# Kernel tuning notes

Measured on AMD Instinct MI355X. Metric: run time of the kernel, lower is better.

The kernel has to match this reference:

```python
import jax, jax.numpy as jnp
import numpy as np

B, T, H, C = 16, 6000, 256, 105
NOTE_BD_TEMP = 1.0
THRESH = 0.5
MIN_GAP = 19      # round(100 * 24000 / 1000 / 128)
REF_GAP = 9       # round(50 * 24000 / 1000 / 128)


def setup_inputs() -> dict:
    key = jax.random.key(0)
    kf, kw = jax.random.split(key)
    feat = jax.random.normal(kf, (B, T, H), dtype=jnp.float32)
    # kaiming normal fan_in: std = sqrt(2/fan_in)
    W = jax.random.normal(kw, (C, H), dtype=jnp.float32) * np.float32(np.sqrt(2.0 / H))
    b = jnp.zeros((C,), dtype=jnp.float32)
    rng = np.random.default_rng(0)
    word_bd = np.zeros((B, T), dtype=np.int32)
    for i in range(B):
        pos = np.cumsum(rng.integers(25, 61, size=T // 25)) + 10
        pos = pos[pos < T - 2]
        word_bd[i, pos] = 1
    lengths = rng.integers(T // 2, T + 1, size=B)
    non_padding = (np.arange(T)[None, :] < lengths[:, None]).astype(np.float32)
    return {"feat": feat, "word_bd": jnp.asarray(word_bd),
            "non_padding": jnp.asarray(non_padding), "W": W, "b": b}


def _phase1(probs, bd):
    # Peak-picking + min-gap merging scan over one sequence.
    # probs, bd: [T]. Returns res: [T+1] int32 (slot T is a dummy write sink).
    def step(carry, inp):
        res, last, start, rmv, rmi = carry
        j, bj, pj = inp
        in_run = start >= 0
        upd = (~in_run) | (pj > rmv)          # running first-argmax of current run
        fin = (~bj) & in_run                  # run just ended at j
        bd_idx = rmi                          # argmax index of the run (== start if len 1)
        merge = fin & (bd_idx - last < MIN_GAP) & (last > 0)
        mid = jnp.round((bd_idx + last).astype(jnp.float32) / 2.0).astype(jnp.int32)
        bd_idx = jnp.where(merge, mid, bd_idx)
        res = res.at[jnp.where(merge, last, T)].set(0)
        res = res.at[jnp.where(fin, bd_idx, T)].set(1)
        last = jnp.where(fin, bd_idx, last)
        start = jnp.where(bj, jnp.where(in_run, start, j), jnp.where(fin, -1, start))
        rmv = jnp.where(bj & upd, pj, rmv)
        rmi = jnp.where(bj & upd, j, rmi)
        return (res, last, start, rmv, rmi), None

    init = (jnp.zeros((T + 1,), jnp.int32), jnp.int32(-1), jnp.int32(-1),
            jnp.float32(-1e30), jnp.int32(0))
    xs = (jnp.arange(T, dtype=jnp.int32), bd, probs)
    (res, _, _, _, _), _ = jax.lax.scan(step, init, xs)
    return res


def _phase2(res, ref):
    # Reconcile predicted boundaries with reference word boundaries.
    ds = jnp.arange(-REF_GAP, REF_GAP)        # window [j-g, j+g-1] == torch slice [j-g : j+g]
    ks = jnp.arange(1, REF_GAP + 1)

    def step(res, j):
        active = ref[j] == 1
        widx = j + ds
        valid = (widx >= 0) & (widx < T)
        cwidx = jnp.clip(widx, 0, T - 1)
        seg = jnp.sum(jnp.where(valid, res[cwidx], 0))
        b0 = seg == 0
        b1 = (seg == 1) & (res[j] != 1)
        b2 = seg > 1
        # branch seg>1: first (in l1,r1,l2,r2,... order) offending boundary to suppress
        lidx = jnp.maximum(0, j - ks)
        ridx = jnp.minimum(T - 1, j + ks)
        cl = (res[lidx] == 1) & (ref[lidx] != 1)
        cr = (res[ridx] == 1) & (ref[ridx] != 1)
        conds = jnp.stack([cl, cr], axis=1).reshape(-1)
        cands = jnp.stack([lidx, ridx], axis=1).reshape(-1)
        zidx = jnp.where(jnp.any(conds), cands[jnp.argmax(conds)], T)
        # apply branch effects (inactive writes go to dummy slot T)
        res = res.at[jnp.where(active & b1 & valid, widx, T)].set(ref[cwidx])
        res = res.at[jnp.where(active & b2, zidx, T)].set(0)
        res = res.at[jnp.where(active & (b0 | b2), j, T)].set(1)
        return res, None

    res, _ = jax.lax.scan(step, res, jnp.arange(T, dtype=jnp.int32))
    return res


def regulate_boundary(bd_logits, word_bd, non_padding):
    probs = jax.nn.sigmoid(bd_logits)
    bd = probs > THRESH
    res = jax.vmap(_phase1)(probs, bd)
    res = jax.vmap(_phase2)(res, word_bd)
    res = res[:, :T]                      # drop dummy slot
    res = res.at[:, 0].set(0)
    L = jnp.sum(non_padding, axis=1).astype(jnp.int32)   # [B]
    keep = jnp.arange(T)[None, :] < (L[:, None] - 1)     # zero out res[i, L-1:]
    return jnp.where(keep, res, 0)


def reference(feat, word_bd, non_padding, W, b):
    # note_head: Linear(H -> C); eval mode so dropout is identity
    logits = jnp.einsum('bth,ch->btc', feat, W) + b           # [B,T,C]
    note_bd_logits = jnp.clip(logits[:, :, 0] / NOTE_BD_TEMP, -16.0, 16.0)
    note_frame_logits = logits[:, :, 1:] / NOTE_BD_TEMP
    note_bd_pred = regulate_boundary(note_bd_logits, word_bd, non_padding)
    return note_bd_logits, note_frame_logits, note_bd_pred
```

## Files before the change

kernel.cpp:

```cpp
#include <hip/hip_runtime.h>

#define NB 16
#define TT 6000
#define HH 256
#define CC 105
#define MIN_GAP_ 19
#define REF_GAP_ 9

using short8  = __attribute__((ext_vector_type(8))) short;
using short4v = __attribute__((ext_vector_type(4))) short;
using f32x4   = __attribute__((ext_vector_type(4))) float;

static __device__ __forceinline__ short f2bf(float x) {
  unsigned u = __builtin_bit_cast(unsigned, x);
  unsigned r = (u + 0x7FFFu + ((u >> 16) & 1u)) >> 16;
  return (short)r;
}

__global__ __launch_bounds__(256) void wconv_kernel(
    const float* __restrict__ W, unsigned short* __restrict__ Wb) {
  const int idx = blockIdx.x * 256 + threadIdx.x;
  const int c = idx >> 8, k = idx & 255;
  const float v = (c < CC - 1) ? W[(size_t)(c + 1) * HH + k] : 0.f;
  Wb[idx] = (unsigned short)f2bf(v);
}

__global__ __launch_bounds__(512, 4) void gemm_mfma(
    const float* __restrict__ feat, const float* __restrict__ W,
    const float* __restrict__ bias, const unsigned short* __restrict__ Wb,
    float* __restrict__ out0, float* __restrict__ out1) {
  __shared__ __align__(16) unsigned short bS[112 * 256];
  const int tid  = threadIdx.x;
  const int wv   = tid >> 6;
  const int lane = tid & 63;
  const int rl   = lane & 15;
  const int kg   = lane >> 4;
  const int row  = blockIdx.x * 128 + wv * 16 + rl;
  const float* frow = feat + (size_t)row * HH;

  short8 breg[7];
#pragma unroll
  for (int i = 0; i < 7; i++)
    breg[i] = *reinterpret_cast<const short8*>(Wb + (((size_t)(i * 512 + tid)) << 3));

  float4 areg[16];
#pragma unroll
  for (int ks = 0; ks < 8; ks++) {
    const int kk = ks * 32 + kg * 8;
    areg[2 * ks]     = *reinterpret_cast<const float4*>(frow + kk);
    areg[2 * ks + 1] = *reinterpret_cast<const float4*>(frow + kk + 4);
  }

#pragma unroll
  for (int i = 0; i < 7; i++) {
    const int byte = (i * 512 + tid) << 4;
    const int brow = byte >> 9;
    const int boff = byte & 511;
    *reinterpret_cast<short8*>(
        (char*)bS + (brow << 9) + (boff ^ ((brow & 7) << 4))) = breg[i];
  }
  __syncthreads();

  const int xr = (rl & 7) << 4;
  f32x4 acc[7];
#pragma unroll
  for (int n = 0; n < 7; n++) acc[n] = (f32x4){0.f, 0.f, 0.f, 0.f};
  float c0 = 0.f;

#pragma unroll
  for (int ks = 0; ks < 8; ks++) {
    const int kk = ks * 32 + kg * 8;
    const float4 a0 = areg[2 * ks];
    const float4 a1 = areg[2 * ks + 1];
    const float4 w0a = *reinterpret_cast<const float4*>(W + kk);
    const float4 w0b = *reinterpret_cast<const float4*>(W + kk + 4);
    c0 = fmaf(a0.x, w0a.x, c0); c0 = fmaf(a0.y, w0a.y, c0);
    c0 = fmaf(a0.z, w0a.z, c0); c0 = fmaf(a0.w, w0a.w, c0);
    c0 = fmaf(a1.x, w0b.x, c0); c0 = fmaf(a1.y, w0b.y, c0);
    c0 = fmaf(a1.z, w0b.z, c0); c0 = fmaf(a1.w, w0b.w, c0);

    short8 av;
    av[0] = f2bf(a0.x); av[1] = f2bf(a0.y); av[2] = f2bf(a0.z); av[3] = f2bf(a0.w);
    av[4] = f2bf(a1.x); av[5] = f2bf(a1.y); av[6] = f2bf(a1.z); av[7] = f2bf(a1.w);

    const int boff = (ks * 64 + kg * 16) ^ xr;
    const char* bbase = (const char*)bS + boff;
    short8 bv[7];
#pragma unroll
    for (int n = 0; n < 7; n++)
      bv[n] = *reinterpret_cast<const short8*>(bbase + ((n * 16 + rl) << 9));
#pragma unroll
    for (int n = 0; n < 7; n++)
      acc[n] = __builtin_amdgcn_mfma_f32_16x16x32_bf16(av, bv[n], acc[n], 0, 0, 0);
  }

  c0 += __shfl_xor(c0, 16);
  c0 += __shfl_xor(c0, 32);
  if (kg == 0) out0[row] = fminf(fmaxf(c0 + bias[0], -16.f), 16.f);

  const int rbase = blockIdx.x * 128 + wv * 16 + kg * 4;
#pragma unroll
  for (int n = 0; n < 7; n++) {
    const int c = n * 16 + rl;
    if (c < CC - 1) {
      const float bb = bias[c + 1];
#pragma unroll
      for (int r = 0; r < 4; r++)
        out1[(size_t)(rbase + r) * (CC - 1) + c] = acc[n][r] + bb;
    }
  }
}

#define NW 192
#define NW_LAST 187
#define CHUNK 32
#define NCLS 19
#define MAXRUNS 3072
#define MAXCH 96

__global__ __launch_bounds__(512) void phase_kernel(
    const float* __restrict__ bd_logits,
    const int* __restrict__ word_bd,
    const float* __restrict__ non_padding,
    float* __restrict__ out2) {
  __shared__ __align__(16) float lbuf[TT];
  __shared__ unsigned char wbuf[TT];
  __shared__ int res[TT];
  __shared__ unsigned bdbits[NW];
  __shared__ int runIdx[MAXRUNS];
  __shared__ int outLast[MAXCH][NCLS + 1];
  __shared__ int chP0[MAXCH];
  __shared__ int inL[MAXCH + 1];
  __shared__ int wsum[8];
  __shared__ int wbase[8];
  __shared__ int L_sh, nruns_sh;

  const int b = blockIdx.x;
  const int tid = threadIdx.x;
  const int lane = tid & 63;
  const int wid = tid >> 6;
  if (tid == 0) L_sh = 0;
  __syncthreads();

  int cnt_np = 0;
#pragma unroll
  for (int k = 0; k < 12; k++) {
    const int j = k * 512 + tid;
    bool pred = false;
    if (j < TT) {
      const float l = bd_logits[(size_t)b * TT + j];
      lbuf[j] = l;
      pred = l > 0.f;
      wbuf[j] = (unsigned char)word_bd[(size_t)b * TT + j];
      res[j] = 0;
      cnt_np += (non_padding[(size_t)b * TT + j] != 0.f) ? 1 : 0;
    }
    const unsigned long long m = __ballot(pred);
    if (lane == 0) {
      const int w0 = (k * 512 + (tid & ~63)) >> 5;
      bdbits[w0]     = (unsigned)m;
      bdbits[w0 + 1] = (unsigned)(m >> 32);
    }
  }
#pragma unroll
  for (int off = 32; off; off >>= 1) cnt_np += __shfl_xor(cnt_np, off);
  if (lane == 0) atomicAdd(&L_sh, cnt_np);
  __syncthreads();

  int cnt = 0;
  unsigned ends = 0;
  if (tid < NW) {
    const unsigned cur = bdbits[tid];
    const unsigned pb = tid ? (bdbits[tid - 1] >> 31) : 0u;
    ends = ((cur << 1) | pb) & ~cur;
    if (tid == NW_LAST) ends &= 0xFFFFu;
    cnt = __popc(ends);
  }
  int v = cnt;
#pragma unroll
  for (int off = 1; off < 64; off <<= 1) {
    const int t = __shfl_up(v, off);
    if (lane >= off) v += t;
  }
  if (lane == 63) wsum[wid] = v;
  __syncthreads();
  if (tid == 0) {
    int s = 0;
#pragma unroll
    for (int w = 0; w < 8; w++) { wbase[w] = s; s += wsum[w]; }
    nruns_sh = s;
  }
  __syncthreads();
  int slot = wbase[wid] + v - cnt;

  if (ends) {
    unsigned m = ends;
    while (m) {
      const int bit = __builtin_ctz(m);
      m &= m - 1;
      const int e = tid * 32 + bit;
      const int eb = e - 1;
      int w = eb >> 5;
      const int bb = eb & 31;
      const unsigned z = bdbits[w] << (31 - bb);
      const unsigned nz = ~z;
      int run = nz ? __builtin_clz(nz) : 32;
      if (run == bb + 1) {
        while (w > 0) {
          w--;
          const unsigned nx = ~bdbits[w];
          const int t2 = nx ? __builtin_clz(nx) : 32;
          run += t2;
          if (t2 < 32) break;
        }
      }
      const int s = e - run;
      float mv = lbuf[s];
      int mi = s;
      for (int i = s + 1; i < e; i++) {
        const float val = lbuf[i];
        if (val > mv) { mv = val; mi = i; }
      }
      runIdx[slot++] = mi;
    }
  }
  __syncthreads();

  const int n = nruns_sh;
  const int nch = (n + CHUNK - 1) / CHUNK;
  for (int f = tid; f < nch * NCLS; f += 512) {
    const int ch = f / NCLS;
    const int cls = f - ch * NCLS;
    const int s = ch * CHUNK;
    const int e = (s + CHUNK < n) ? s + CHUNK : n;
    const int p0 = runIdx[s];
    if (cls == NCLS - 1) chP0[ch] = p0;
    int last = (cls < 18) ? (p0 - 18 + cls) : -1;
    for (int i = s; i < e; i++) {
      int bd = runIdx[i];
      if (last > 0 && bd - last < MIN_GAP_) {
        const int sum = bd + last;
        const int h = sum >> 1;
        bd = (sum & 1) ? (h + (h & 1)) : h;
      }
      last = bd;
    }
    outLast[ch][cls] = last;
  }
  __syncthreads();

  if (wid == 0) {
    int q = -1;
    int row = (lane < NCLS && nch > 0) ? outLast[0][lane] : -1;
    for (int ch = 0; ch < nch; ch++) {
      const int rown = (lane < NCLS && ch + 1 < nch) ? outLast[ch + 1][lane] : -1;
      const int p0 = chP0[ch];
      const int cls = (q > 0 && p0 - q < MIN_GAP_) ? (q - (p0 - 18)) : (NCLS - 1);
      if (lane == 0) inL[ch] = q;
      q = __shfl(row, cls);
      row = rown;
    }
    if (lane == 0) inL[nch] = q;
  }
  __syncthreads();

  for (int ch = tid; ch < nch; ch += 512) {
    const int s = ch * CHUNK;
    const int e = (s + CHUNK < n) ? s + CHUNK : n;
    const int qin = inL[ch];
    const int qout = inL[ch + 1];
    if (qin >= 0 && qin != qout) res[qin] = 1;
    int last = qin;
    for (int i = s; i < e; i++) {
      int bd = runIdx[i];
      if (last > 0 && bd - last < MIN_GAP_) {
        const int sum = bd + last;
        const int h = sum >> 1;
        bd = (sum & 1) ? (h + (h & 1)) : h;
        if (last != qout) res[last] = 0;
      }
      if (bd != qout) res[bd] = 1;
      last = bd;
    }
  }
  if (tid == 0 && n > 0) res[inL[nch]] = 1;
  __syncthreads();

  for (int j = tid; j < TT; j += 512) {
    if (wbuf[j] != 1) continue;
    const int lo = (j - REF_GAP_ < 0) ? 0 : j - REF_GAP_;
    const int hi = (j + REF_GAP_ - 1 > TT - 1) ? TT - 1 : j + REF_GAP_ - 1;
    int seg = 0;
    for (int w = lo; w <= hi; w++) seg += res[w];
    if (seg == 0) {
      res[j] = 1;
    } else if (seg == 1) {
      if (res[j] != 1) {
        for (int w = lo; w <= hi; w++) res[w] = (int)wbuf[w];
      }
    } else {
      int zidx = -1;
      for (int k = 1; k <= REF_GAP_; k++) {
        const int li = (j - k < 0) ? 0 : j - k;
        const int ri = (j + k > TT - 1) ? TT - 1 : j + k;
        if (res[li] == 1 && wbuf[li] != 1) { zidx = li; break; }
        if (res[ri] == 1 && wbuf[ri] != 1) { zidx = ri; break; }
      }
      if (zidx >= 0) res[zidx] = 0;
      res[j] = 1;
    }
  }
  __syncthreads();

  const int L = L_sh;
  for (int t = tid; t < TT; t += 512)
    out2[(size_t)b * TT + t] = (t >= 1 && t < L - 1) ? (float)res[t] : 0.f;
}

extern "C" void kernel_launch(void* const* d_in, const int* in_sizes, int n_in,
                              void* d_out, int out_size, void* d_ws, size_t ws_size,
                              hipStream_t stream) {
  const float* feat        = (const float*)d_in[0];
  const int*   word_bd     = (const int*)d_in[1];
  const float* non_padding = (const float*)d_in[2];
  const float* W           = (const float*)d_in[3];
  const float* bias        = (const float*)d_in[4];

  float* out  = (float*)d_out;
  float* out0 = out;
  float* out1 = out + (size_t)NB * TT;
  float* out2 = out + (size_t)NB * TT + (size_t)NB * TT * (CC - 1);

  unsigned short* Wb = (unsigned short*)d_ws;

  hipLaunchKernelGGL(wconv_kernel, dim3(112), dim3(256), 0, stream, W, Wb);
  hipLaunchKernelGGL(gemm_mfma, dim3((NB * TT) / 128), dim3(512), 0, stream,
                     feat, W, bias, Wb, out0, out1);
  hipLaunchKernelGGL(phase_kernel, dim3(NB), dim3(512), 0, stream,
                     out0, word_bd, non_padding, out2);
}
```

Measured before the change: 69.67 us.

## Widen phase kernel to 1024 threads and map merge chunks to wavefronts

The phase kernel now runs 1024 threads per block. The chunked merge scans assign one wavefront per chunk: the chunk's run indices are loaded into lanes once and broadcast with shuffles, instead of every thread rereading shared memory serially. The intent is to cut shared-memory latency in the serial chunk loops and spread the load/refine loops across more threads. The GEMM grid is written as a named constant equal to the old value, so that part is cosmetic. In exchange, each chunk's sequential loop now runs in lockstep across a full wavefront, and a 1024-thread block may be limited in register use.

After: 81.84 us. +17.5%, slower.

```diff
diff --git a/kernel.cpp b/kernel.cpp
--- a/kernel.cpp
+++ b/kernel.cpp
@@ -24,6 +24,8 @@
   const float v = (c < CC - 1) ? W[(size_t)(c + 1) * HH + k] : 0.f;
   Wb[idx] = (unsigned short)f2bf(v);
 }
+
+#define NGRID 750
 
 __global__ __launch_bounds__(512, 4) void gemm_mfma(
     const float* __restrict__ feat, const float* __restrict__ W,
@@ -118,7 +120,7 @@
 #define MAXRUNS 3072
 #define MAXCH 96
 
-__global__ __launch_bounds__(512) void phase_kernel(
+__global__ __launch_bounds__(1024) void phase_kernel(
     const float* __restrict__ bd_logits,
     const int* __restrict__ word_bd,
     const float* __restrict__ non_padding,
@@ -131,21 +133,21 @@
   __shared__ int outLast[MAXCH][NCLS + 1];
   __shared__ int chP0[MAXCH];
   __shared__ int inL[MAXCH + 1];
-  __shared__ int wsum[8];
-  __shared__ int wbase[8];
+  __shared__ int wsum[16];
+  __shared__ int wbase[16];
   __shared__ int L_sh, nruns_sh;
 
   const int b = blockIdx.x;
   const int tid = threadIdx.x;
   const int lane = tid & 63;
-  const int wid = tid >> 6;
+  const int wv = tid >> 6;
   if (tid == 0) L_sh = 0;
   __syncthreads();
 
   int cnt_np = 0;
 #pragma unroll
-  for (int k = 0; k < 12; k++) {
-    const int j = k * 512 + tid;
+  for (int k = 0; k < 6; k++) {
+    const int j = k * 1024 + tid;
     bool pred = false;
     if (j < TT) {
       const float l = bd_logits[(size_t)b * TT + j];
@@ -157,7 +159,7 @@
     }
     const unsigned long long m = __ballot(pred);
     if (lane == 0) {
-      const int w0 = (k * 512 + (tid & ~63)) >> 5;
+      const int w0 = (k * 1024 + (tid & ~63)) >> 5;
       bdbits[w0]     = (unsigned)m;
       bdbits[w0 + 1] = (unsigned)(m >> 32);
     }
@@ -182,16 +184,16 @@
     const int t = __shfl_up(v, off);
     if (lane >= off) v += t;
   }
-  if (lane == 63) wsum[wid] = v;
+  if (lane == 63) wsum[wv] = v;
   __syncthreads();
   if (tid == 0) {
     int s = 0;
 #pragma unroll
-    for (int w = 0; w < 8; w++) { wbase[w] = s; s += wsum[w]; }
+    for (int w = 0; w < 16; w++) { wbase[w] = s; s += wsum[w]; }
     nruns_sh = s;
   }
   __syncthreads();
-  int slot = wbase[wid] + v - cnt;
+  int slot = wbase[wv] + v - cnt;
 
   if (ends) {
     unsigned m = ends;
@@ -228,16 +230,16 @@
 
   const int n = nruns_sh;
   const int nch = (n + CHUNK - 1) / CHUNK;
-  for (int f = tid; f < nch * NCLS; f += 512) {
-    const int ch = f / NCLS;
-    const int cls = f - ch * NCLS;
+  for (int ch = wv; ch < nch; ch += 16) {
     const int s = ch * CHUNK;
     const int e = (s + CHUNK < n) ? s + CHUNK : n;
-    const int p0 = runIdx[s];
-    if (cls == NCLS - 1) chP0[ch] = p0;
-    int last = (cls < 18) ? (p0 - 18 + cls) : -1;
-    for (int i = s; i < e; i++) {
-      int bd = runIdx[i];
+    const int m = e - s;
+    const int myrun = (lane < m) ? runIdx[s + lane] : 0;
+    const int p0 = __shfl(myrun, 0);
+    if (lane == 0) chP0[ch] = p0;
+    int last = (lane < 18) ? (p0 - 18 + lane) : -1;
+    for (int i = 0; i < m; i++) {
+      int bd = __shfl(myrun, i);
       if (last > 0 && bd - last < MIN_GAP_) {
         const int sum = bd + last;
         const int h = sum >> 1;
@@ -245,11 +247,11 @@
       }
       last = bd;
     }
-    outLast[ch][cls] = last;
-  }
-  __syncthreads();
-
-  if (wid == 0) {
+    if (lane < NCLS) outLast[ch][lane] = last;
+  }
+  __syncthreads();
+
+  if (wv == 0) {
     int q = -1;
     int row = (lane < NCLS && nch > 0) ? outLast[0][lane] : -1;
     for (int ch = 0; ch < nch; ch++) {
@@ -264,29 +266,32 @@
   }
   __syncthreads();
 
-  for (int ch = tid; ch < nch; ch += 512) {
+  for (int ch = wv; ch < nch; ch += 16) {
     const int s = ch * CHUNK;
     const int e = (s + CHUNK < n) ? s + CHUNK : n;
+    const int m = e - s;
+    const int myrun = (lane < m) ? runIdx[s + lane] : 0;
     const int qin = inL[ch];
     const int qout = inL[ch + 1];
-    if (qin >= 0 && qin != qout) res[qin] = 1;
+    if (lane == 0 && qin >= 0 && qin != qout) res[qin] = 1;
     int last = qin;
-    for (int i = s; i < e; i++) {
-      int bd = runIdx[i];
-      if (last > 0 && bd - last < MIN_GAP_) {
+    for (int i = 0; i < m; i++) {
+      int bd = __shfl(myrun, i);
+      const bool mg = (last > 0 && bd - last < MIN_GAP_);
+      if (mg) {
         const int sum = bd + last;
         const int h = sum >> 1;
         bd = (sum & 1) ? (h + (h & 1)) : h;
-        if (last != qout) res[last] = 0;
-      }
-      if (bd != qout) res[bd] = 1;
+        if (lane == i && last != qout) res[last] = 0;
+      }
+      if (lane == i && bd != qout) res[bd] = 1;
       last = bd;
     }
   }
   if (tid == 0 && n > 0) res[inL[nch]] = 1;
   __syncthreads();
 
-  for (int j = tid; j < TT; j += 512) {
+  for (int j = tid; j < TT; j += 1024) {
     if (wbuf[j] != 1) continue;
     const int lo = (j - REF_GAP_ < 0) ? 0 : j - REF_GAP_;
     const int hi = (j + REF_GAP_ - 1 > TT - 1) ? TT - 1 : j + REF_GAP_ - 1;
@@ -313,7 +318,7 @@
   __syncthreads();
 
   const int L = L_sh;
-  for (int t = tid; t < TT; t += 512)
+  for (int t = tid; t < TT; t += 1024)
     out2[(size_t)b * TT + t] = (t >= 1 && t < L - 1) ? (float)res[t] : 0.f;
 }
 
@@ -334,8 +339,8 @@
   unsigned short* Wb = (unsigned short*)d_ws;
 
   hipLaunchKernelGGL(wconv_kernel, dim3(112), dim3(256), 0, stream, W, Wb);
-  hipLaunchKernelGGL(gemm_mfma, dim3((NB * TT) / 128), dim3(512), 0, stream,
+  hipLaunchKernelGGL(gemm_mfma, dim3(NGRID), dim3(512), 0, stream,
                      feat, W, bias, Wb, out0, out1);
-  hipLaunchKernelGGL(phase_kernel, dim3(NB), dim3(512), 0, stream,
+  hipLaunchKernelGGL(phase_kernel, dim3(NB), dim3(1024), 0, stream,
                      out0, word_bd, non_padding, out2);
 }
```
